# Performance work log

Hardware: AMD Instinct MI355X
Metric: run time of the kernel (lower is better)

## Reference

```python
import jax, jax.numpy as jnp
import numpy as np

HEADS = 4

def _pair_msg(H, w2, B, xsrc):
    # H:[E,mid] radial-MLP hidden; w2:[mid,co,ci,nf]; B:[E,m_out,m_in,nf] CG/SH basis; xsrc:[E,ci,m_in]
    tmp = jnp.einsum('epqf,eiq->eipf', B, xsrc)          # basis-weighted input  [E,ci,m_out,nf]
    R = jnp.einsum('eh,hoif->eoif', H, w2)               # per-edge radial weights [E,co,ci,nf]
    return jnp.einsum('eoif,eipf->eop', R, tmp)          # edge message [E,co,m_out]

def _conv_edges(ef, w1, w2_nf1, w2_11, b00, b01, b10, b11, x0s, x1s):
    # pair index p = 2*d_in + d_out; pairs (0,0),(0,1),(1,0) have nf=1, pair (1,1) has nf=3
    H = jax.nn.relu(jnp.einsum('ef,pfh->peh', ef, w1))
    m0 = _pair_msg(H[0], w2_nf1[0][..., None], b00, x0s) + _pair_msg(H[2], w2_nf1[2][..., None], b10, x1s)
    m1 = _pair_msg(H[1], w2_nf1[1][..., None], b01, x0s) + _pair_msg(H[3], w2_11, b11, x1s)
    return m0, m1

def _seg_softmax(z, dst, n):
    m = jax.ops.segment_max(z, dst, num_segments=n)
    m = jnp.where(jnp.isfinite(m), m, 0.0)
    e = jnp.exp(z - m[dst])
    s = jax.ops.segment_sum(e, dst, num_segments=n)
    return e / (s[dst] + 1e-9)

def _norm_se3(x, g, b, eps=1e-3):
    n = jnp.sqrt((x * x).sum(-1) + 1e-12)                # per-channel irrep norm [N,C]
    mu = n.mean(-1, keepdims=True)
    var = ((n - mu) ** 2).mean(-1, keepdims=True)
    ln = (n - mu) / jnp.sqrt(var + 1e-5) * g + b
    return x * (jax.nn.relu(ln) / (n + eps))[..., None]

def _forward(x0, x1, edge_feat, b00, b01, b10, b11, kv_w1, kv_w2_nf1, kv_w2_11,
             wq, wproj, norm_gamma, norm_beta, fc_w1, fc_w2_nf1, fc_w2_11, fc_wself,
             edge_src, edge_dst):
    N = x0.shape[0]
    E = edge_src.shape[0]
    L = kv_w1.shape[0]
    ckv = wq.shape[-1]
    scale = 1.0 / np.sqrt((ckv // HEADS) * 4)            # key feats per head over degrees 0,1 (1+3 comps)
    hs = lambda t: t.reshape(t.shape[0], HEADS, ckv // HEADS, t.shape[-1])
    for l in range(L):
        # AttentionBlockSE3: ConvSE3 -> per-edge key/value; LinearSE3 -> query; seg-softmax attention
        kv0, kv1 = _conv_edges(edge_feat, kv_w1[l], kv_w2_nf1[l], kv_w2_11[l],
                               b00, b01, b10, b11, x0[edge_src], x1[edge_src])
        k0, v0 = kv0[:, :ckv], kv0[:, ckv:]
        k1, v1 = kv1[:, :ckv], kv1[:, ckv:]
        q0 = jnp.einsum('ncm,cd->ndm', x0, wq[l, 0])
        q1 = jnp.einsum('ncm,cd->ndm', x1, wq[l, 1])
        z = (hs(q0)[edge_dst] * hs(k0)).sum((2, 3)) + (hs(q1)[edge_dst] * hs(k1)).sum((2, 3))
        alpha = _seg_softmax(z * scale, edge_dst, N)     # [E,heads]
        a0 = (alpha[:, :, None, None] * hs(v0)).reshape(E, ckv, 1)
        a1 = (alpha[:, :, None, None] * hs(v1)).reshape(E, ckv, 3)
        o0 = jax.ops.segment_sum(a0, edge_dst, num_segments=N)
        o1 = jax.ops.segment_sum(a1, edge_dst, num_segments=N)
        # project concat(attn_out, skip) per degree, then NormSE3
        x0 = jnp.einsum('ncm,cd->ndm', jnp.concatenate([o0, x0], 1), wproj[l, 0])
        x1 = jnp.einsum('ncm,cd->ndm', jnp.concatenate([o1, x1], 1), wproj[l, 1])
        x0 = _norm_se3(x0, norm_gamma[l, 0], norm_beta[l, 0])
        x1 = _norm_se3(x1, norm_gamma[l, 1], norm_beta[l, 1])
    # final ConvSE3 with self-interaction, scatter-aggregated over dst nodes
    m0, m1 = _conv_edges(edge_feat, fc_w1, fc_w2_nf1, fc_w2_11,
                         b00, b01, b10, b11, x0[edge_src], x1[edge_src])
    y0 = jax.ops.segment_sum(m0, edge_dst, num_segments=N) + jnp.einsum('ncm,cd->ndm', x0, fc_wself[0])
    y1 = jax.ops.segment_sum(m1, edge_dst, num_segments=N) + jnp.einsum('ncm,cd->ndm', x1, fc_wself[1])
    return jnp.concatenate([y0.reshape(N, -1), y1.reshape(N, -1)], axis=1)

def setup_inputs() -> dict:
    key = jax.random.key(0)
    ks = jax.random.split(key, 20)
    N, E, C, L = 8192, 131072, 16, 2
    Fe, mid, KV, ckv, Co = 16, 16, 16, 8, 8
    f = lambda k, s, sc=1.0: jax.random.normal(k, s, dtype=jnp.float32) * sc
    return {
        'x0': f(ks[0], (N, C, 1)),
        'x1': f(ks[1], (N, C, 3)),
        'edge_feat': f(ks[2], (E, Fe)),
        'b00': f(ks[3], (E, 1, 1, 1)),
        'b01': f(ks[4], (E, 3, 1, 1)),
        'b10': f(ks[5], (E, 1, 3, 1)),
        'b11': f(ks[6], (E, 3, 3, 3)),
        'kv_w1': f(ks[7], (L, 4, Fe, mid), 0.1),
        'kv_w2_nf1': f(ks[8], (L, 3, mid, KV, C), 0.1),
        'kv_w2_11': f(ks[9], (L, mid, KV, C, 3), 0.1),
        'wq': f(ks[10], (L, 2, C, ckv), 0.1),
        'wproj': f(ks[11], (L, 2, ckv + C, C), 0.1),
        'norm_gamma': jnp.ones((L, 2, C), dtype=jnp.float32),
        'norm_beta': jnp.zeros((L, 2, C), dtype=jnp.float32),
        'fc_w1': f(ks[12], (4, Fe, mid), 0.1),
        'fc_w2_nf1': f(ks[13], (3, mid, Co, C), 0.1),
        'fc_w2_11': f(ks[14], (mid, Co, C, 3), 0.1),
        'fc_wself': f(ks[15], (2, C, Co), 0.1),
        'edge_src': jax.random.randint(ks[16], (E,), 0, N, dtype=jnp.int32),
        'edge_dst': jax.random.randint(ks[17], (E,), 0, N, dtype=jnp.int32),
    }

def reference(x0, x1, edge_feat, b00, b01, b10, b11, kv_w1, kv_w2_nf1, kv_w2_11,
              wq, wproj, norm_gamma, norm_beta, fc_w1, fc_w2_nf1, fc_w2_11, fc_wself,
              edge_src, edge_dst):
    return _forward(x0, x1, edge_feat, b00, b01, b10, b11, kv_w1, kv_w2_nf1, kv_w2_11,
                    wq, wproj, norm_gamma, norm_beta, fc_w1, fc_w2_nf1, fc_w2_11, fc_wself,
                    edge_src, edge_dst)
```

## Files before the change

### kernel.cpp

```cpp
#include <hip/hip_runtime.h>
#include <hip/hip_bf16.h>
#include <math.h>


typedef short short8 __attribute__((ext_vector_type(8)));
typedef float f32x4 __attribute__((ext_vector_type(4)));

union ABfrag {
    short8 s8;
    __hip_bfloat162 b2[4];
};

static __device__ __forceinline__ unsigned short f2bf(float f) {
    unsigned x = __float_as_uint(f);
    unsigned r = x + 0x7FFFu + ((x >> 16) & 1u);
    return (unsigned short)(r >> 16);
}

__global__ void k_zero(int* p, int n) {
    int i = blockIdx.x * 256 + threadIdx.x;
    if (i < n) p[i] = 0;
}

__global__ void k_hist(const int* __restrict__ dst, int* __restrict__ counts, int E) {
    int e = blockIdx.x * 256 + threadIdx.x;
    if (e < E) atomicAdd(&counts[dst[e]], 1);
}

__global__ __launch_bounds__(1024) void k_scan(const int* __restrict__ counts,
                                               int* __restrict__ rowptr,
                                               int* __restrict__ cursor,
                                               int N, int CH) {
    __shared__ int part[1024];
    int t = threadIdx.x;
    int s = 0;
    for (int i = 0; i < CH; ++i) {
        int idx = t * CH + i;
        if (idx < N) s += counts[idx];
    }
    part[t] = s;
    __syncthreads();
    for (int off = 1; off < 1024; off <<= 1) {
        int v = (t >= off) ? part[t - off] : 0;
        __syncthreads();
        part[t] += v;
        __syncthreads();
    }
    int run = (t == 0) ? 0 : part[t - 1];
    for (int i = 0; i < CH; ++i) {
        int idx = t * CH + i;
        if (idx < N) {
            rowptr[idx] = run;
            cursor[idx] = run;
            run += counts[idx];
        }
    }
    if (t == 0) rowptr[N] = part[1023];
}

__global__ void k_scatter(const int* __restrict__ dst, int* __restrict__ cursor,
                          int* __restrict__ eids, int E) {
    int e = blockIdx.x * 256 + threadIdx.x;
    if (e < E) {
        int pos = atomicAdd(&cursor[dst[e]], 1);
        eids[pos] = e;
    }
}

__global__ void k_initx(const float* __restrict__ x0, const float* __restrict__ x1,
                        float* __restrict__ xs0, float* __restrict__ xs1, int n0, int n1) {
    int i = blockIdx.x * 256 + threadIdx.x;
    if (i < n0) xs0[i] = x0[i];
    else if (i < n0 + n1) xs1[i - n0] = x1[i - n0];
}

__global__ void k_efb(const float* __restrict__ ef, unsigned short* __restrict__ efb, int n) {
    int i = blockIdx.x * 256 + threadIdx.x;
    if (i < n) efb[i] = f2bf(ef[i]);
}

__global__ void k_prepw(const float* __restrict__ kvw1, const float* __restrict__ fcw1,
                        const float* __restrict__ kvw2n, const float* __restrict__ kvw211,
                        const float* __restrict__ fcw2n, const float* __restrict__ fcw211,
                        unsigned short* __restrict__ Wfrag) {
    int t = blockIdx.x * 256 + threadIdx.x;
    if (t >= 156 * 64 * 8) return;
    int j = t & 7;
    int lane = (t >> 3) & 63;
    int row = t >> 9;
    int quad = lane >> 4, m = lane & 15;
    int c = row / 52, r = row % 52;
    int KVO = (c < 2) ? 16 : 8;
    const float* w1src = (c < 2) ? (kvw1 + c * 1024) : fcw1;
    const float* w2n = (c < 2) ? (kvw2n + c * 12288) : fcw2n;
    const float* w211 = (c < 2) ? (kvw211 + c * 12288) : fcw211;
    float v = 0.f;
    if (r < 4) {
        if (quad < 2) v = w1src[r * 256 + (quad * 8 + j) * 16 + m];
    } else if (r < 28) {
        int fam = (r - 4) >> 3, kk = (r - 4) & 7;
        int h = quad * 4 + (j & 3), i = 2 * kk + (j >> 2);
        if (m < KVO) v = w2n[((fam * 16 + h) * KVO + m) * 16 + i];
    } else {
        int kk = r - 28;
        int h = quad * 4 + (j & 3);
        int ifx = 2 * kk + (j >> 2);
        int i = ifx / 3, f = ifx % 3;
        if (m < KVO) v = w211[((h * KVO + m) * 16 + i) * 3 + f];
    }
    Wfrag[t] = f2bf(v);
}

template <int KVO, bool DO_Z>
__global__ __launch_bounds__(256) void k_conv(
    int E,
    const int* __restrict__ src, const int* __restrict__ dst,
    const float* __restrict__ xs0, const float* __restrict__ xs1,
    const float* __restrict__ b00, const float* __restrict__ b01,
    const float* __restrict__ b10, const float* __restrict__ b11,
    const unsigned short* __restrict__ efb,
    const unsigned short* __restrict__ Wfrag,
    int base,
    const float* __restrict__ q0, const float* __restrict__ q1,
    float* __restrict__ out0, float* __restrict__ out1, float* __restrict__ zb)
{
    __shared__ float xBL[4][16 * 148];
    int tid = threadIdx.x;
    int wave = tid >> 6, lane = tid & 63;
    int tile = blockIdx.x * 4 + wave;
    if (tile * 16 >= E) return;
    int m = lane & 15, quad = lane >> 4;
    int e0 = tile * 16;
    int me = e0 + m;
    int s = src[me];
    float* xw = xBL[wave];
    const short8* W8 = (const short8*)Wfrag;

    {
        float x1c[12];
        const float4* xp = (const float4*)(xs1 + (size_t)s * 48 + quad * 12);
#pragma unroll
        for (int cc = 0; cc < 3; ++cc) {
            float4 v = xp[cc];
            x1c[cc * 4 + 0] = v.x; x1c[cc * 4 + 1] = v.y;
            x1c[cc * 4 + 2] = v.z; x1c[cc * 4 + 3] = v.w;
        }
        float b11r[27];
#pragma unroll
        for (int k = 0; k < 27; ++k) b11r[k] = b11[(size_t)me * 27 + k];
#pragma unroll
        for (int p = 0; p < 3; ++p) {
            float vals[12];
#pragma unroll
            for (int i2 = 0; i2 < 4; ++i2) {
#pragma unroll
                for (int f = 0; f < 3; ++f) {
                    float a = 0.f;
#pragma unroll
                    for (int q = 0; q < 3; ++q) a += x1c[i2 * 3 + q] * b11r[p * 9 + q * 3 + f];
                    vals[i2 * 3 + f] = a;
                }
            }
#pragma unroll
            for (int cc = 0; cc < 3; ++cc) {
                float4 v = make_float4(vals[cc * 4 + 0], vals[cc * 4 + 1],
                                       vals[cc * 4 + 2], vals[cc * 4 + 3]);
                *(float4*)&xw[m * 148 + p * 48 + quad * 12 + cc * 4] = v;
            }
        }
    }
    __syncthreads();

    float x0r[16];
    {
        const float4* p = (const float4*)(xs0 + (size_t)s * 16);
#pragma unroll
        for (int k = 0; k < 4; ++k) {
            float4 v = p[k];
            x0r[k * 4 + 0] = v.x; x0r[k * 4 + 1] = v.y;
            x0r[k * 4 + 2] = v.z; x0r[k * 4 + 3] = v.w;
        }
    }
    float t10[16];
    {
        float bq0 = b10[(size_t)me * 3 + 0], bq1 = b10[(size_t)me * 3 + 1],
              bq2 = b10[(size_t)me * 3 + 2];
        const float4* xp = (const float4*)(xs1 + (size_t)s * 48);
#pragma unroll
        for (int g = 0; g < 4; ++g) {
            float4 a = xp[g * 3 + 0], b = xp[g * 3 + 1], cc = xp[g * 3 + 2];
            float xf[12] = {a.x, a.y, a.z, a.w, b.x, b.y, b.z, b.w, cc.x, cc.y, cc.z, cc.w};
#pragma unroll
            for (int i2 = 0; i2 < 4; ++i2)
                t10[g * 4 + i2] = bq0 * xf[i2 * 3] + bq1 * xf[i2 * 3 + 1] + bq2 * xf[i2 * 3 + 2];
        }
    }

    float Hp[4][4];
    {
        short8 efr = {0, 0, 0, 0, 0, 0, 0, 0};
        if (quad < 2) efr = *(const short8*)(efb + (size_t)me * 16 + quad * 8);
        f32x4 z4 = {0.f, 0.f, 0.f, 0.f};
#pragma unroll
        for (int pp = 0; pp < 4; ++pp) {
            short8 w1f = W8[(size_t)(base + pp) * 64 + lane];
            f32x4 hacc = __builtin_amdgcn_mfma_f32_16x16x32_bf16(w1f, efr, z4, 0, 0, 0);
#pragma unroll
            for (int r = 0; r < 4; ++r) Hp[pp][r] = fmaxf(hacc[r], 0.f);
        }
    }

    f32x4 acc0 = {0.f, 0.f, 0.f, 0.f}, acc1 = acc0, acc2 = acc0;
    f32x4 accP0 = acc0, accP1 = acc0, accP2 = acc0;

#pragma unroll
    for (int kk = 0; kk < 8; ++kk) {
        float xa = x0r[2 * kk], xb_ = x0r[2 * kk + 1];
        float ta = t10[2 * kk], tb_ = t10[2 * kk + 1];
        ABfrag a0, a1, a2;
        a0.b2[0] = __float22bfloat162_rn(make_float2(Hp[0][0] * xa, Hp[0][1] * xa));
        a0.b2[1] = __float22bfloat162_rn(make_float2(Hp[0][2] * xa, Hp[0][3] * xa));
        a0.b2[2] = __float22bfloat162_rn(make_float2(Hp[0][0] * xb_, Hp[0][1] * xb_));
        a0.b2[3] = __float22bfloat162_rn(make_float2(Hp[0][2] * xb_, Hp[0][3] * xb_));
        a1.b2[0] = __float22bfloat162_rn(make_float2(Hp[1][0] * xa, Hp[1][1] * xa));
        a1.b2[1] = __float22bfloat162_rn(make_float2(Hp[1][2] * xa, Hp[1][3] * xa));
        a1.b2[2] = __float22bfloat162_rn(make_float2(Hp[1][0] * xb_, Hp[1][1] * xb_));
        a1.b2[3] = __float22bfloat162_rn(make_float2(Hp[1][2] * xb_, Hp[1][3] * xb_));
        a2.b2[0] = __float22bfloat162_rn(make_float2(Hp[2][0] * ta, Hp[2][1] * ta));
        a2.b2[1] = __float22bfloat162_rn(make_float2(Hp[2][2] * ta, Hp[2][3] * ta));
        a2.b2[2] = __float22bfloat162_rn(make_float2(Hp[2][0] * tb_, Hp[2][1] * tb_));
        a2.b2[3] = __float22bfloat162_rn(make_float2(Hp[2][2] * tb_, Hp[2][3] * tb_));
        short8 w0 = W8[(size_t)(base + 4 + kk) * 64 + lane];
        short8 w1f = W8[(size_t)(base + 4 + 8 + kk) * 64 + lane];
        short8 w2f = W8[(size_t)(base + 4 + 16 + kk) * 64 + lane];
        acc0 = __builtin_amdgcn_mfma_f32_16x16x32_bf16(w0, a0.s8, acc0, 0, 0, 0);
        acc1 = __builtin_amdgcn_mfma_f32_16x16x32_bf16(w1f, a1.s8, acc1, 0, 0, 0);
        acc2 = __builtin_amdgcn_mfma_f32_16x16x32_bf16(w2f, a2.s8, acc2, 0, 0, 0);
    }

#pragma unroll
    for (int kko = 0; kko < 12; ++kko) {
        float4 xb0 = *(const float4*)&xw[m * 148 + 0 * 48 + 4 * kko];
        float4 xb1 = *(const float4*)&xw[m * 148 + 1 * 48 + 4 * kko];
        float4 xb2 = *(const float4*)&xw[m * 148 + 2 * 48 + 4 * kko];
        float x0a[4] = {xb0.x, xb0.y, xb0.z, xb0.w};
        float x1a[4] = {xb1.x, xb1.y, xb1.z, xb1.w};
        float x2a[4] = {xb2.x, xb2.y, xb2.z, xb2.w};
#pragma unroll
        for (int t = 0; t < 2; ++t) {
            float p0a = x0a[2 * t], p0b = x0a[2 * t + 1];
            float p1a = x1a[2 * t], p1b = x1a[2 * t + 1];
            float p2a = x2a[2 * t], p2b = x2a[2 * t + 1];
            ABfrag a0, a1, a2;
            a0.b2[0] = __float22bfloat162_rn(make_float2(Hp[3][0] * p0a, Hp[3][1] * p0a));
            a0.b2[1] = __float22bfloat162_rn(make_float2(Hp[3][2] * p0a, Hp[3][3] * p0a));
            a0.b2[2] = __float22bfloat162_rn(make_float2(Hp[3][0] * p0b, Hp[3][1] * p0b));
            a0.b2[3] = __float22bfloat162_rn(make_float2(Hp[3][2] * p0b, Hp[3][3] * p0b));
            a1.b2[0] = __float22bfloat162_rn(make_float2(Hp[3][0] * p1a, Hp[3][1] * p1a));
            a1.b2[1] = __float22bfloat162_rn(make_float2(Hp[3][2] * p1a, Hp[3][3] * p1a));
            a1.b2[2] = __float22bfloat162_rn(make_float2(Hp[3][0] * p1b, Hp[3][1] * p1b));
            a1.b2[3] = __float22bfloat162_rn(make_float2(Hp[3][2] * p1b, Hp[3][3] * p1b));
            a2.b2[0] = __float22bfloat162_rn(make_float2(Hp[3][0] * p2a, Hp[3][1] * p2a));
            a2.b2[1] = __float22bfloat162_rn(make_float2(Hp[3][2] * p2a, Hp[3][3] * p2a));
            a2.b2[2] = __float22bfloat162_rn(make_float2(Hp[3][0] * p2b, Hp[3][1] * p2b));
            a2.b2[3] = __float22bfloat162_rn(make_float2(Hp[3][2] * p2b, Hp[3][3] * p2b));
            short8 wf = W8[(size_t)(base + 28 + 2 * kko + t) * 64 + lane];
            accP0 = __builtin_amdgcn_mfma_f32_16x16x32_bf16(wf, a0.s8, accP0, 0, 0, 0);
            accP1 = __builtin_amdgcn_mfma_f32_16x16x32_bf16(wf, a1.s8, accP1, 0, 0, 0);
            accP2 = __builtin_amdgcn_mfma_f32_16x16x32_bf16(wf, a2.s8, accP2, 0, 0, 0);
        }
    }

    float b00r = b00[me];
    float b01r0 = b01[(size_t)me * 3 + 0], b01r1 = b01[(size_t)me * 3 + 1],
          b01r2 = b01[(size_t)me * 3 + 2];
    float o0v[4], o1v[4][3];
#pragma unroll
    for (int r = 0; r < 4; ++r) {
        o0v[r] = b00r * acc0[r] + acc2[r];
        o1v[r][0] = b01r0 * acc1[r] + accP0[r];
        o1v[r][1] = b01r1 * acc1[r] + accP1[r];
        o1v[r][2] = b01r2 * acc1[r] + accP2[r];
    }
    bool doStore = DO_Z ? (quad >= 2) : (quad * 4 < KVO);
    if (doStore) {
        *(float4*)&out0[(size_t)me * KVO + quad * 4] =
            make_float4(o0v[0], o0v[1], o0v[2], o0v[3]);
        float* p1 = out1 + ((size_t)me * KVO + quad * 4) * 3;
        *(float4*)&p1[0] = make_float4(o1v[0][0], o1v[0][1], o1v[0][2], o1v[1][0]);
        *(float4*)&p1[4] = make_float4(o1v[1][1], o1v[1][2], o1v[2][0], o1v[2][1]);
        *(float4*)&p1[8] = make_float4(o1v[2][2], o1v[3][0], o1v[3][1], o1v[3][2]);
    }
    if (DO_Z && quad < 2) {
        int n = dst[me];
        float4 q0v = *(const float4*)&q0[(size_t)n * 8 + quad * 4];
        const float4* q1p = (const float4*)&q1[(size_t)n * 24 + quad * 12];
        float4 qa = q1p[0], qb = q1p[1], qc = q1p[2];
        float q1f[12] = {qa.x, qa.y, qa.z, qa.w, qb.x, qb.y, qb.z, qb.w,
                         qc.x, qc.y, qc.z, qc.w};
        float q0f[4] = {q0v.x, q0v.y, q0v.z, q0v.w};
        float zh0 = 0.f, zh1 = 0.f;
#pragma unroll
        for (int r = 0; r < 4; ++r) {
            float tt = q0f[r] * o0v[r] + q1f[r * 3 + 0] * o1v[r][0] +
                       q1f[r * 3 + 1] * o1v[r][1] + q1f[r * 3 + 2] * o1v[r][2];
            if (r < 2) zh0 += tt;
            else zh1 += tt;
        }
        const float scale = 0.35355339059327373f;
        *(float2*)&zb[(size_t)me * 4 + quad * 2] = make_float2(zh0 * scale, zh1 * scale);
    }
}

__global__ void k_q(int N, const float* __restrict__ xs0, const float* __restrict__ xs1,
                    const float* __restrict__ wq,
                    float* __restrict__ q0, float* __restrict__ q1) {
    int t = blockIdx.x * 256 + threadIdx.x;
    if (t >= N * 32) return;
    int n = t >> 5, comp = t & 31;
    if (comp < 8) {
        float a = 0.f;
#pragma unroll
        for (int c = 0; c < 16; ++c) a += xs0[n * 16 + c] * wq[c * 8 + comp];
        q0[n * 8 + comp] = a;
    } else {
        int idx = comp - 8, dd = idx / 3, mm = idx % 3;
        float a = 0.f;
#pragma unroll
        for (int c = 0; c < 16; ++c) a += xs1[n * 48 + c * 3 + mm] * wq[128 + c * 8 + dd];
        q1[n * 24 + dd * 3 + mm] = a;
    }
}

__global__ __launch_bounds__(256) void k_attn(
    int N,
    const int* __restrict__ rowptr, const int* __restrict__ eids,
    const float* __restrict__ z, const float* __restrict__ kv0, const float* __restrict__ kv1,
    const float* __restrict__ wproj,
    const float* __restrict__ gamma, const float* __restrict__ beta,
    float* __restrict__ xs0, float* __restrict__ xs1) {
    __shared__ float wpL[768];
    __shared__ float gL[32], btL[32];
    __shared__ float inb[16][100];
    int tid = threadIdx.x;
    for (int i = tid; i < 768; i += 256) wpL[i] = wproj[i];
    if (tid < 32) { gL[tid] = gamma[tid]; btL[tid] = beta[tid]; }
    int wave = tid >> 6, lane = tid & 63;
    int sub = lane >> 4, l16 = lane & 15;
    int nodeIdx = wave * 4 + sub;
    int n = blockIdx.x * 16 + nodeIdx;
    if (n >= N) n = N - 1;
    int base = rowptr[n], deg = rowptr[n + 1] - base;

    float mx0 = -INFINITY, mx1 = -INFINITY, mx2 = -INFINITY, mx3 = -INFINITY;
    for (int j = l16; j < deg; j += 16) {
        int e = eids[base + j];
        float4 zv = *(const float4*)&z[e * 4];
        mx0 = fmaxf(mx0, zv.x); mx1 = fmaxf(mx1, zv.y);
        mx2 = fmaxf(mx2, zv.z); mx3 = fmaxf(mx3, zv.w);
    }
#pragma unroll
    for (int off = 1; off < 16; off <<= 1) {
        mx0 = fmaxf(mx0, __shfl_xor(mx0, off));
        mx1 = fmaxf(mx1, __shfl_xor(mx1, off));
        mx2 = fmaxf(mx2, __shfl_xor(mx2, off));
        mx3 = fmaxf(mx3, __shfl_xor(mx3, off));
    }
    if (!isfinite(mx0)) mx0 = 0.f;
    if (!isfinite(mx1)) mx1 = 0.f;
    if (!isfinite(mx2)) mx2 = 0.f;
    if (!isfinite(mx3)) mx3 = 0.f;

    float s0 = 0.f, s1 = 0.f, s2 = 0.f, s3 = 0.f;
    for (int j = l16; j < deg; j += 16) {
        int e = eids[base + j];
        float4 zv = *(const float4*)&z[e * 4];
        s0 += __expf(zv.x - mx0); s1 += __expf(zv.y - mx1);
        s2 += __expf(zv.z - mx2); s3 += __expf(zv.w - mx3);
    }
#pragma unroll
    for (int off = 1; off < 16; off <<= 1) {
        s0 += __shfl_xor(s0, off); s1 += __shfl_xor(s1, off);
        s2 += __shfl_xor(s2, off); s3 += __shfl_xor(s3, off);
    }
    float mxa[4] = {mx0, mx1, mx2, mx3};
    float inva[4] = {1.f / (s0 + 1e-9f), 1.f / (s1 + 1e-9f),
                     1.f / (s2 + 1e-9f), 1.f / (s3 + 1e-9f)};

    int c0 = l16, c1 = l16 + 16;
    int kkA = c0 >> 3, dA = c0 & 7, hA = dA >> 1;
    int kkB = c1 >> 3, dB = c1 & 7, hB = dB >> 1;
    float mA = mxa[hA], iA = inva[hA];
    float mB = mxa[hB], iB = inva[hB];
    float accA = 0.f, accB = 0.f;
    for (int j = 0; j < deg; ++j) {
        int e = eids[base + j];
        float wA = __expf(z[e * 4 + hA] - mA) * iA;
        float wB = __expf(z[e * 4 + hB] - mB) * iB;
        float vA = (kkA == 0) ? kv0[(size_t)e * 16 + 8 + dA]
                              : kv1[((size_t)e * 16 + 8 + dA) * 3 + (kkA - 1)];
        float vB = kv1[((size_t)e * 16 + 8 + dB) * 3 + (kkB - 1)];
        accA += wA * vA;
        accB += wB * vB;
    }

    float* in0 = inb[nodeIdx];
    float* in1 = in0 + 24;
    if (c0 < 8) in0[c0] = accA;
    else in1[dA * 3 + (kkA - 1)] = accA;
    in1[dB * 3 + (kkB - 1)] = accB;
    in0[8 + l16] = xs0[(size_t)n * 16 + l16];
    {
        const float* xp = xs1 + (size_t)n * 48 + l16 * 3;
        in1[24 + l16 * 3 + 0] = xp[0];
        in1[24 + l16 * 3 + 1] = xp[1];
        in1[24 + l16 * 3 + 2] = xp[2];
    }
    __syncthreads();

    int c = l16;
    float y0 = 0.f;
#pragma unroll
    for (int j = 0; j < 24; ++j) y0 += in0[j] * wpL[j * 16 + c];
    float y1v[3];
#pragma unroll
    for (int mm = 0; mm < 3; ++mm) {
        float y = 0.f;
#pragma unroll
        for (int j = 0; j < 24; ++j) y += in1[j * 3 + mm] * wpL[384 + j * 16 + c];
        y1v[mm] = y;
    }
    float n0 = sqrtf(y0 * y0 + 1e-12f);
    float n1 = sqrtf(y1v[0] * y1v[0] + y1v[1] * y1v[1] + y1v[2] * y1v[2] + 1e-12f);
    float mu0 = n0, mu1 = n1;
#pragma unroll
    for (int off = 1; off < 16; off <<= 1) {
        mu0 += __shfl_xor(mu0, off);
        mu1 += __shfl_xor(mu1, off);
    }
    mu0 *= 0.0625f; mu1 *= 0.0625f;
    float dv0 = n0 - mu0, dv1 = n1 - mu1;
    float var0 = dv0 * dv0, var1 = dv1 * dv1;
#pragma unroll
    for (int off = 1; off < 16; off <<= 1) {
        var0 += __shfl_xor(var0, off);
        var1 += __shfl_xor(var1, off);
    }
    var0 *= 0.0625f; var1 *= 0.0625f;
    float ln0 = dv0 * rsqrtf(var0 + 1e-5f) * gL[c] + btL[c];
    float ln1 = dv1 * rsqrtf(var1 + 1e-5f) * gL[16 + c] + btL[16 + c];
    float fac0 = fmaxf(ln0, 0.f) / (n0 + 1e-3f);
    float fac1 = fmaxf(ln1, 0.f) / (n1 + 1e-3f);
    xs0[(size_t)n * 16 + c] = y0 * fac0;
    float* xo = xs1 + (size_t)n * 48 + c * 3;
    xo[0] = y1v[0] * fac1;
    xo[1] = y1v[1] * fac1;
    xo[2] = y1v[2] * fac1;
}

__global__ __launch_bounds__(256) void k_out(
    int N,
    const int* __restrict__ rowptr, const int* __restrict__ eids,
    const float* __restrict__ m0f, const float* __restrict__ m1f,
    const float* __restrict__ xs0, const float* __restrict__ xs1,
    const float* __restrict__ wself,
    float* __restrict__ out) {
    int tid = threadIdx.x;
    int wave = tid >> 6, lane = tid & 63;
    int sub = lane >> 4, l16 = lane & 15;
    int n = blockIdx.x * 16 + wave * 4 + sub;
    if (n >= N) n = N - 1;
    int base = rowptr[n], deg = rowptr[n + 1] - base;

    int c0 = l16, c1 = l16 + 16;
    int kkA = c0 >> 3, dA = c0 & 7;
    int kkB = c1 >> 3, dB = c1 & 7;
    float accA = 0.f, accB = 0.f;
    for (int j = 0; j < deg; ++j) {
        int e = eids[base + j];
        accA += (kkA == 0) ? m0f[(size_t)e * 8 + dA]
                           : m1f[((size_t)e * 8 + dA) * 3 + (kkA - 1)];
        accB += m1f[((size_t)e * 8 + dB) * 3 + (kkB - 1)];
    }
    if (kkA == 0) {
#pragma unroll
        for (int c = 0; c < 16; ++c) accA += xs0[(size_t)n * 16 + c] * wself[c * 8 + dA];
    } else {
#pragma unroll
        for (int c = 0; c < 16; ++c)
            accA += xs1[(size_t)n * 48 + c * 3 + (kkA - 1)] * wself[128 + c * 8 + dA];
    }
    {
        int mm = kkB - 1;
#pragma unroll
        for (int c = 0; c < 16; ++c)
            accB += xs1[(size_t)n * 48 + c * 3 + mm] * wself[128 + c * 8 + dB];
    }
    out[(size_t)n * 32 + ((kkA == 0) ? dA : (8 + dA * 3 + (kkA - 1)))] = accA;
    out[(size_t)n * 32 + (8 + dB * 3 + (kkB - 1))] = accB;
}

extern "C" void kernel_launch(void* const* d_in, const int* in_sizes, int n_in,
                              void* d_out, int out_size, void* d_ws, size_t ws_size,
                              hipStream_t stream) {
    const float* x0 = (const float*)d_in[0];
    const float* x1 = (const float*)d_in[1];
    const float* ef = (const float*)d_in[2];
    const float* b00 = (const float*)d_in[3];
    const float* b01 = (const float*)d_in[4];
    const float* b10 = (const float*)d_in[5];
    const float* b11 = (const float*)d_in[6];
    const float* kvw1 = (const float*)d_in[7];
    const float* kvw2n = (const float*)d_in[8];
    const float* kvw211 = (const float*)d_in[9];
    const float* wq = (const float*)d_in[10];
    const float* wproj = (const float*)d_in[11];
    const float* gam = (const float*)d_in[12];
    const float* bet = (const float*)d_in[13];
    const float* fcw1 = (const float*)d_in[14];
    const float* fcw2n = (const float*)d_in[15];
    const float* fcw211 = (const float*)d_in[16];
    const float* fcself = (const float*)d_in[17];
    const int* esrc = (const int*)d_in[18];
    const int* edst = (const int*)d_in[19];
    int N = in_sizes[0] / 16;
    int E = in_sizes[18];
    float* out = (float*)d_out;

    float* ws = (float*)d_ws;
    size_t off = 0;
    float* xs0 = ws + off; off += (size_t)N * 16;
    float* xs1 = ws + off; off += (size_t)N * 48;
    float* q0b = ws + off; off += (size_t)N * 8;
    float* q1b = ws + off; off += (size_t)N * 24;
    float* kv0 = ws + off; off += (size_t)E * 16;
    float* kv1 = ws + off; off += (size_t)E * 48;
    float* zb = ws + off; off += (size_t)E * 4;
    int* counts = (int*)(ws + off); off += N;
    int* rowptr = (int*)(ws + off); off += N + 1;
    int* cursor = (int*)(ws + off); off += N;
    int* eids = (int*)(ws + off); off += E;
    off = (off + 3) & ~(size_t)3;
    unsigned short* efb = (unsigned short*)(ws + off); off += (size_t)E * 16 / 2;
    unsigned short* Wfrag = (unsigned short*)(ws + off); off += (size_t)156 * 64 * 8 / 2;

    const int tpb = 256;
    int ebl = (E + 255) / 256;
    int cblk = (E / 16 + 3) / 4;
    int nbl16 = (N + 15) / 16;

    k_prepw<<<(156 * 512 + 255) / 256, tpb, 0, stream>>>(kvw1, fcw1, kvw2n, kvw211,
                                                         fcw2n, fcw211, Wfrag);
    k_efb<<<(E * 16 + 255) / 256, tpb, 0, stream>>>(ef, efb, E * 16);
    k_zero<<<(N + 255) / 256, tpb, 0, stream>>>(counts, N);
    k_hist<<<ebl, tpb, 0, stream>>>(edst, counts, E);
    int CH = (N + 1023) / 1024;
    k_scan<<<1, 1024, 0, stream>>>(counts, rowptr, cursor, N, CH);
    k_scatter<<<ebl, tpb, 0, stream>>>(edst, cursor, eids, E);
    k_initx<<<(N * 64 + 255) / 256, tpb, 0, stream>>>(x0, x1, xs0, xs1, N * 16, N * 48);

    for (int l = 0; l < 2; ++l) {
        k_q<<<(N * 32 + 255) / 256, tpb, 0, stream>>>(N, xs0, xs1, wq + l * 256, q0b, q1b);
        k_conv<16, true><<<cblk, tpb, 0, stream>>>(E, esrc, edst, xs0, xs1, b00, b01, b10, b11,
                                                   efb, Wfrag, l * 52, q0b, q1b, kv0, kv1, zb);
        k_attn<<<nbl16, tpb, 0, stream>>>(N, rowptr, eids, zb, kv0, kv1,
                                          wproj + l * 768, gam + l * 32, bet + l * 32, xs0, xs1);
    }
    k_conv<8, false><<<cblk, tpb, 0, stream>>>(E, esrc, edst, xs0, xs1, b00, b01, b10, b11,
                                               efb, Wfrag, 2 * 52, q0b, q1b, kv0, kv1, zb);
    k_out<<<nbl16, tpb, 0, stream>>>(N, rowptr, eids, kv0, kv1, xs0, xs1, fcself, out);
}
```

Measured before the change: 354.4 us.

## Switch conv to fp16 packed math and store values in dst-sorted rows

The conv kernel now builds its MFMA operands with packed fp16 multiplies and f16 MFMA instead of fp32 multiplies followed by bf16 conversion. It also writes only the value part of each message into a CSR-ordered 32-float row per edge, using a per-edge position from the scatter step. The attention and output kernels therefore read contiguous rows with no edge-id indirection, and attention stages its softmax weights in shared memory. Small setup kernels are merged and a memset replaces the zero kernel. fp16 has a narrower range than bf16, so values could overflow or lose precision.

```diff
diff --git a/kernel.cpp b/kernel.cpp
--- a/kernel.cpp
+++ b/kernel.cpp
@@ -1,26 +1,19 @@
 #include <hip/hip_runtime.h>
-#include <hip/hip_bf16.h>
+#include <hip/hip_fp16.h>
 #include <math.h>
 
 
-typedef short short8 __attribute__((ext_vector_type(8)));
+typedef _Float16 half8 __attribute__((ext_vector_type(8)));
 typedef float f32x4 __attribute__((ext_vector_type(4)));
 
-union ABfrag {
-    short8 s8;
-    __hip_bfloat162 b2[4];
+union AF {
+    half8 h8;
+    __half2 h2[4];
 };
-
-static __device__ __forceinline__ unsigned short f2bf(float f) {
-    unsigned x = __float_as_uint(f);
-    unsigned r = x + 0x7FFFu + ((x >> 16) & 1u);
-    return (unsigned short)(r >> 16);
-}
-
-__global__ void k_zero(int* p, int n) {
-    int i = blockIdx.x * 256 + threadIdx.x;
-    if (i < n) p[i] = 0;
-}
+union U32h2 {
+    unsigned u;
+    __half2 h;
+};
 
 __global__ void k_hist(const int* __restrict__ dst, int* __restrict__ counts, int E) {
     int e = blockIdx.x * 256 + threadIdx.x;
@@ -59,24 +52,25 @@
 }
 
 __global__ void k_scatter(const int* __restrict__ dst, int* __restrict__ cursor,
-                          int* __restrict__ eids, int E) {
+                          int* __restrict__ pose, int E) {
     int e = blockIdx.x * 256 + threadIdx.x;
     if (e < E) {
         int pos = atomicAdd(&cursor[dst[e]], 1);
-        eids[pos] = e;
-    }
-}
-
-__global__ void k_initx(const float* __restrict__ x0, const float* __restrict__ x1,
-                        float* __restrict__ xs0, float* __restrict__ xs1, int n0, int n1) {
+        pose[e] = pos;
+    }
+}
+
+__global__ void k_misc(const float* __restrict__ x0, const float* __restrict__ x1,
+                       const float* __restrict__ ef,
+                       float* __restrict__ xs0, float* __restrict__ xs1,
+                       unsigned short* __restrict__ efh, int n0, int n1, int n2) {
     int i = blockIdx.x * 256 + threadIdx.x;
     if (i < n0) xs0[i] = x0[i];
     else if (i < n0 + n1) xs1[i - n0] = x1[i - n0];
-}
-
-__global__ void k_efb(const float* __restrict__ ef, unsigned short* __restrict__ efb, int n) {
-    int i = blockIdx.x * 256 + threadIdx.x;
-    if (i < n) efb[i] = f2bf(ef[i]);
+    else if (i < n0 + n1 + n2) {
+        int k = i - n0 - n1;
+        efh[k] = __half_as_ushort(__float2half(ef[k]));
+    }
 }
 
 __global__ void k_prepw(const float* __restrict__ kvw1, const float* __restrict__ fcw1,
@@ -108,23 +102,24 @@
         int i = ifx / 3, f = ifx % 3;
         if (m < KVO) v = w211[((h * KVO + m) * 16 + i) * 3 + f];
     }
-    Wfrag[t] = f2bf(v);
+    Wfrag[t] = __half_as_ushort(__float2half(v));
 }
 
 template <int KVO, bool DO_Z>
 __global__ __launch_bounds__(256) void k_conv(
     int E,
     const int* __restrict__ src, const int* __restrict__ dst,
+    const int* __restrict__ pose,
     const float* __restrict__ xs0, const float* __restrict__ xs1,
     const float* __restrict__ b00, const float* __restrict__ b01,
     const float* __restrict__ b10, const float* __restrict__ b11,
-    const unsigned short* __restrict__ efb,
+    const unsigned short* __restrict__ efh,
     const unsigned short* __restrict__ Wfrag,
-    int base,
+    int wbase,
     const float* __restrict__ q0, const float* __restrict__ q1,
-    float* __restrict__ out0, float* __restrict__ out1, float* __restrict__ zb)
+    float* __restrict__ vrow, float* __restrict__ zb)
 {
-    __shared__ float xBL[4][16 * 148];
+    __shared__ unsigned xBL[4][16 * 148];
     int tid = threadIdx.x;
     int wave = tid >> 6, lane = tid & 63;
     int tile = blockIdx.x * 4 + wave;
@@ -133,8 +128,8 @@
     int e0 = tile * 16;
     int me = e0 + m;
     int s = src[me];
-    float* xw = xBL[wave];
-    const short8* W8 = (const short8*)Wfrag;
+    unsigned* xw = xBL[wave];
+    const half8* W8 = (const half8*)Wfrag;
 
     {
         float x1c[12];
@@ -163,26 +158,31 @@
             }
 #pragma unroll
             for (int cc = 0; cc < 3; ++cc) {
-                float4 v = make_float4(vals[cc * 4 + 0], vals[cc * 4 + 1],
-                                       vals[cc * 4 + 2], vals[cc * 4 + 3]);
-                *(float4*)&xw[m * 148 + p * 48 + quad * 12 + cc * 4] = v;
+                unsigned uu[4];
+#pragma unroll
+                for (int i3 = 0; i3 < 4; ++i3) {
+                    U32h2 u;
+                    u.h = __float2half2_rn(vals[cc * 4 + i3]);
+                    uu[i3] = u.u;
+                }
+                *(uint4*)&xw[m * 148 + p * 48 + quad * 12 + cc * 4] =
+                    make_uint4(uu[0], uu[1], uu[2], uu[3]);
             }
         }
     }
     __syncthreads();
 
-    float x0r[16];
+    __half2 x0d[16], t10d[16];
     {
         const float4* p = (const float4*)(xs0 + (size_t)s * 16);
 #pragma unroll
         for (int k = 0; k < 4; ++k) {
             float4 v = p[k];
-            x0r[k * 4 + 0] = v.x; x0r[k * 4 + 1] = v.y;
-            x0r[k * 4 + 2] = v.z; x0r[k * 4 + 3] = v.w;
-        }
-    }
-    float t10[16];
-    {
+            x0d[k * 4 + 0] = __float2half2_rn(v.x);
+            x0d[k * 4 + 1] = __float2half2_rn(v.y);
+            x0d[k * 4 + 2] = __float2half2_rn(v.z);
+            x0d[k * 4 + 3] = __float2half2_rn(v.w);
+        }
         float bq0 = b10[(size_t)me * 3 + 0], bq1 = b10[(size_t)me * 3 + 1],
               bq2 = b10[(size_t)me * 3 + 2];
         const float4* xp = (const float4*)(xs1 + (size_t)s * 48);
@@ -192,21 +192,24 @@
             float xf[12] = {a.x, a.y, a.z, a.w, b.x, b.y, b.z, b.w, cc.x, cc.y, cc.z, cc.w};
 #pragma unroll
             for (int i2 = 0; i2 < 4; ++i2)
-                t10[g * 4 + i2] = bq0 * xf[i2 * 3] + bq1 * xf[i2 * 3 + 1] + bq2 * xf[i2 * 3 + 2];
-        }
-    }
-
-    float Hp[4][4];
+                t10d[g * 4 + i2] = __float2half2_rn(
+                    bq0 * xf[i2 * 3] + bq1 * xf[i2 * 3 + 1] + bq2 * xf[i2 * 3 + 2]);
+        }
+    }
+
+    __half2 Hp2[4][2];
     {
-        short8 efr = {0, 0, 0, 0, 0, 0, 0, 0};
-        if (quad < 2) efr = *(const short8*)(efb + (size_t)me * 16 + quad * 8);
+        half8 efr = {0, 0, 0, 0, 0, 0, 0, 0};
+        if (quad < 2) efr = *(const half8*)(efh + (size_t)me * 16 + quad * 8);
         f32x4 z4 = {0.f, 0.f, 0.f, 0.f};
 #pragma unroll
         for (int pp = 0; pp < 4; ++pp) {
-            short8 w1f = W8[(size_t)(base + pp) * 64 + lane];
-            f32x4 hacc = __builtin_amdgcn_mfma_f32_16x16x32_bf16(w1f, efr, z4, 0, 0, 0);
-#pragma unroll
-            for (int r = 0; r < 4; ++r) Hp[pp][r] = fmaxf(hacc[r], 0.f);
+            half8 w1f = W8[(size_t)(wbase + pp) * 64 + lane];
+            f32x4 hacc = __builtin_amdgcn_mfma_f32_16x16x32_f16(w1f, efr, z4, 0, 0, 0);
+            Hp2[pp][0] = __float22half2_rn(
+                make_float2(fmaxf(hacc[0], 0.f), fmaxf(hacc[1], 0.f)));
+            Hp2[pp][1] = __float22half2_rn(
+                make_float2(fmaxf(hacc[2], 0.f), fmaxf(hacc[3], 0.f)));
         }
     }
 
@@ -215,59 +218,49 @@
 
 #pragma unroll
     for (int kk = 0; kk < 8; ++kk) {
-        float xa = x0r[2 * kk], xb_ = x0r[2 * kk + 1];
-        float ta = t10[2 * kk], tb_ = t10[2 * kk + 1];
-        ABfrag a0, a1, a2;
-        a0.b2[0] = __float22bfloat162_rn(make_float2(Hp[0][0] * xa, Hp[0][1] * xa));
-        a0.b2[1] = __float22bfloat162_rn(make_float2(Hp[0][2] * xa, Hp[0][3] * xa));
-        a0.b2[2] = __float22bfloat162_rn(make_float2(Hp[0][0] * xb_, Hp[0][1] * xb_));
-        a0.b2[3] = __float22bfloat162_rn(make_float2(Hp[0][2] * xb_, Hp[0][3] * xb_));
-        a1.b2[0] = __float22bfloat162_rn(make_float2(Hp[1][0] * xa, Hp[1][1] * xa));
-        a1.b2[1] = __float22bfloat162_rn(make_float2(Hp[1][2] * xa, Hp[1][3] * xa));
-        a1.b2[2] = __float22bfloat162_rn(make_float2(Hp[1][0] * xb_, Hp[1][1] * xb_));
-        a1.b2[3] = __float22bfloat162_rn(make_float2(Hp[1][2] * xb_, Hp[1][3] * xb_));
-        a2.b2[0] = __float22bfloat162_rn(make_float2(Hp[2][0] * ta, Hp[2][1] * ta));
-        a2.b2[1] = __float22bfloat162_rn(make_float2(Hp[2][2] * ta, Hp[2][3] * ta));
-        a2.b2[2] = __float22bfloat162_rn(make_float2(Hp[2][0] * tb_, Hp[2][1] * tb_));
-        a2.b2[3] = __float22bfloat162_rn(make_float2(Hp[2][2] * tb_, Hp[2][3] * tb_));
-        short8 w0 = W8[(size_t)(base + 4 + kk) * 64 + lane];
-        short8 w1f = W8[(size_t)(base + 4 + 8 + kk) * 64 + lane];
-        short8 w2f = W8[(size_t)(base + 4 + 16 + kk) * 64 + lane];
-        acc0 = __builtin_amdgcn_mfma_f32_16x16x32_bf16(w0, a0.s8, acc0, 0, 0, 0);
-        acc1 = __builtin_amdgcn_mfma_f32_16x16x32_bf16(w1f, a1.s8, acc1, 0, 0, 0);
-        acc2 = __builtin_amdgcn_mfma_f32_16x16x32_bf16(w2f, a2.s8, acc2, 0, 0, 0);
+        __half2 xA = x0d[2 * kk], xB = x0d[2 * kk + 1];
+        __half2 tA = t10d[2 * kk], tB = t10d[2 * kk + 1];
+        AF a0, a1, a2;
+        a0.h2[0] = __hmul2(Hp2[0][0], xA); a0.h2[1] = __hmul2(Hp2[0][1], xA);
+        a0.h2[2] = __hmul2(Hp2[0][0], xB); a0.h2[3] = __hmul2(Hp2[0][1], xB);
+        a1.h2[0] = __hmul2(Hp2[1][0], xA); a1.h2[1] = __hmul2(Hp2[1][1], xA);
+        a1.h2[2] = __hmul2(Hp2[1][0], xB); a1.h2[3] = __hmul2(Hp2[1][1], xB);
+        a2.h2[0] = __hmul2(Hp2[2][0], tA); a2.h2[1] = __hmul2(Hp2[2][1], tA);
+        a2.h2[2] = __hmul2(Hp2[2][0], tB); a2.h2[3] = __hmul2(Hp2[2][1], tB);
+        half8 w0 = W8[(size_t)(wbase + 4 + kk) * 64 + lane];
+        half8 w1f = W8[(size_t)(wbase + 12 + kk) * 64 + lane];
+        half8 w2f = W8[(size_t)(wbase + 20 + kk) * 64 + lane];
+        acc0 = __builtin_amdgcn_mfma_f32_16x16x32_f16(w0, a0.h8, acc0, 0, 0, 0);
+        acc1 = __builtin_amdgcn_mfma_f32_16x16x32_f16(w1f, a1.h8, acc1, 0, 0, 0);
+        acc2 = __builtin_amdgcn_mfma_f32_16x16x32_f16(w2f, a2.h8, acc2, 0, 0, 0);
     }
 
 #pragma unroll
     for (int kko = 0; kko < 12; ++kko) {
-        float4 xb0 = *(const float4*)&xw[m * 148 + 0 * 48 + 4 * kko];
-        float4 xb1 = *(const float4*)&xw[m * 148 + 1 * 48 + 4 * kko];
-        float4 xb2 = *(const float4*)&xw[m * 148 + 2 * 48 + 4 * kko];
-        float x0a[4] = {xb0.x, xb0.y, xb0.z, xb0.w};
-        float x1a[4] = {xb1.x, xb1.y, xb1.z, xb1.w};
-        float x2a[4] = {xb2.x, xb2.y, xb2.z, xb2.w};
+        uint4 xu0 = *(const uint4*)&xw[m * 148 + 0 * 48 + 4 * kko];
+        uint4 xu1 = *(const uint4*)&xw[m * 148 + 1 * 48 + 4 * kko];
+        uint4 xu2 = *(const uint4*)&xw[m * 148 + 2 * 48 + 4 * kko];
+        unsigned qa0[4] = {xu0.x, xu0.y, xu0.z, xu0.w};
+        unsigned qa1[4] = {xu1.x, xu1.y, xu1.z, xu1.w};
+        unsigned qa2[4] = {xu2.x, xu2.y, xu2.z, xu2.w};
 #pragma unroll
         for (int t = 0; t < 2; ++t) {
-            float p0a = x0a[2 * t], p0b = x0a[2 * t + 1];
-            float p1a = x1a[2 * t], p1b = x1a[2 * t + 1];
-            float p2a = x2a[2 * t], p2b = x2a[2 * t + 1];
-            ABfrag a0, a1, a2;
-            a0.b2[0] = __float22bfloat162_rn(make_float2(Hp[3][0] * p0a, Hp[3][1] * p0a));
-            a0.b2[1] = __float22bfloat162_rn(make_float2(Hp[3][2] * p0a, Hp[3][3] * p0a));
-            a0.b2[2] = __float22bfloat162_rn(make_float2(Hp[3][0] * p0b, Hp[3][1] * p0b));
-            a0.b2[3] = __float22bfloat162_rn(make_float2(Hp[3][2] * p0b, Hp[3][3] * p0b));
-            a1.b2[0] = __float22bfloat162_rn(make_float2(Hp[3][0] * p1a, Hp[3][1] * p1a));
-            a1.b2[1] = __float22bfloat162_rn(make_float2(Hp[3][2] * p1a, Hp[3][3] * p1a));
-            a1.b2[2] = __float22bfloat162_rn(make_float2(Hp[3][0] * p1b, Hp[3][1] * p1b));
-            a1.b2[3] = __float22bfloat162_rn(make_float2(Hp[3][2] * p1b, Hp[3][3] * p1b));
-            a2.b2[0] = __float22bfloat162_rn(make_float2(Hp[3][0] * p2a, Hp[3][1] * p2a));
-            a2.b2[1] = __float22bfloat162_rn(make_float2(Hp[3][2] * p2a, Hp[3][3] * p2a));
-            a2.b2[2] = __float22bfloat162_rn(make_float2(Hp[3][0] * p2b, Hp[3][1] * p2b));
-            a2.b2[3] = __float22bfloat162_rn(make_float2(Hp[3][2] * p2b, Hp[3][3] * p2b));
-            short8 wf = W8[(size_t)(base + 28 + 2 * kko + t) * 64 + lane];
-            accP0 = __builtin_amdgcn_mfma_f32_16x16x32_bf16(wf, a0.s8, accP0, 0, 0, 0);
-            accP1 = __builtin_amdgcn_mfma_f32_16x16x32_bf16(wf, a1.s8, accP1, 0, 0, 0);
-            accP2 = __builtin_amdgcn_mfma_f32_16x16x32_bf16(wf, a2.s8, accP2, 0, 0, 0);
+            U32h2 u;
+            __half2 p0a, p0b, p1a, p1b, p2a, p2b;
+            u.u = qa0[2 * t]; p0a = u.h; u.u = qa0[2 * t + 1]; p0b = u.h;
+            u.u = qa1[2 * t]; p1a = u.h; u.u = qa1[2 * t + 1]; p1b = u.h;
+            u.u = qa2[2 * t]; p2a = u.h; u.u = qa2[2 * t + 1]; p2b = u.h;
+            AF a0, a1, a2;
+            a0.h2[0] = __hmul2(Hp2[3][0], p0a); a0.h2[1] = __hmul2(Hp2[3][1], p0a);
+            a0.h2[2] = __hmul2(Hp2[3][0], p0b); a0.h2[3] = __hmul2(Hp2[3][1], p0b);
+            a1.h2[0] = __hmul2(Hp2[3][0], p1a); a1.h2[1] = __hmul2(Hp2[3][1], p1a);
+            a1.h2[2] = __hmul2(Hp2[3][0], p1b); a1.h2[3] = __hmul2(Hp2[3][1], p1b);
+            a2.h2[0] = __hmul2(Hp2[3][0], p2a); a2.h2[1] = __hmul2(Hp2[3][1], p2a);
+            a2.h2[2] = __hmul2(Hp2[3][0], p2b); a2.h2[3] = __hmul2(Hp2[3][1], p2b);
+            half8 wf = W8[(size_t)(wbase + 28 + 2 * kko + t) * 64 + lane];
+            accP0 = __builtin_amdgcn_mfma_f32_16x16x32_f16(wf, a0.h8, accP0, 0, 0, 0);
+            accP1 = __builtin_amdgcn_mfma_f32_16x16x32_f16(wf, a1.h8, accP1, 0, 0, 0);
+            accP2 = __builtin_amdgcn_mfma_f32_16x16x32_f16(wf, a2.h8, accP2, 0, 0, 0);
         }
     }
 
@@ -282,11 +275,13 @@
         o1v[r][1] = b01r1 * acc1[r] + accP1[r];
         o1v[r][2] = b01r2 * acc1[r] + accP2[r];
     }
-    bool doStore = DO_Z ? (quad >= 2) : (quad * 4 < KVO);
+    int pos = pose[me];
+    bool doStore = DO_Z ? (quad >= 2) : (quad < 2);
     if (doStore) {
-        *(float4*)&out0[(size_t)me * KVO + quad * 4] =
-            make_float4(o0v[0], o0v[1], o0v[2], o0v[3]);
-        float* p1 = out1 + ((size_t)me * KVO + quad * 4) * 3;
+        int qa = DO_Z ? (quad - 2) : quad;
+        float* vp = vrow + (size_t)pos * 32;
+        *(float4*)&vp[qa * 4] = make_float4(o0v[0], o0v[1], o0v[2], o0v[3]);
+        float* p1 = vp + 8 + qa * 12;
         *(float4*)&p1[0] = make_float4(o1v[0][0], o1v[0][1], o1v[0][2], o1v[1][0]);
         *(float4*)&p1[4] = make_float4(o1v[1][1], o1v[1][2], o1v[2][0], o1v[2][1]);
         *(float4*)&p1[8] = make_float4(o1v[2][2], o1v[3][0], o1v[3][1], o1v[3][2]);
@@ -295,9 +290,9 @@
         int n = dst[me];
         float4 q0v = *(const float4*)&q0[(size_t)n * 8 + quad * 4];
         const float4* q1p = (const float4*)&q1[(size_t)n * 24 + quad * 12];
-        float4 qa = q1p[0], qb = q1p[1], qc = q1p[2];
-        float q1f[12] = {qa.x, qa.y, qa.z, qa.w, qb.x, qb.y, qb.z, qb.w,
-                         qc.x, qc.y, qc.z, qc.w};
+        float4 qa4 = q1p[0], qb4 = q1p[1], qc4 = q1p[2];
+        float q1f[12] = {qa4.x, qa4.y, qa4.z, qa4.w, qb4.x, qb4.y, qb4.z, qb4.w,
+                         qc4.x, qc4.y, qc4.z, qc4.w};
         float q0f[4] = {q0v.x, q0v.y, q0v.z, q0v.w};
         float zh0 = 0.f, zh1 = 0.f;
 #pragma unroll
@@ -308,7 +303,7 @@
             else zh1 += tt;
         }
         const float scale = 0.35355339059327373f;
-        *(float2*)&zb[(size_t)me * 4 + quad * 2] = make_float2(zh0 * scale, zh1 * scale);
+        *(float2*)&zb[(size_t)pos * 4 + quad * 2] = make_float2(zh0 * scale, zh1 * scale);
     }
 }
 
@@ -334,14 +329,15 @@
 
 __global__ __launch_bounds__(256) void k_attn(
     int N,
-    const int* __restrict__ rowptr, const int* __restrict__ eids,
-    const float* __restrict__ z, const float* __restrict__ kv0, const float* __restrict__ kv1,
+    const int* __restrict__ rowptr,
+    const float* __restrict__ zb, const float* __restrict__ vrow,
     const float* __restrict__ wproj,
     const float* __restrict__ gamma, const float* __restrict__ beta,
     float* __restrict__ xs0, float* __restrict__ xs1) {
     __shared__ float wpL[768];
     __shared__ float gL[32], btL[32];
     __shared__ float inb[16][100];
+    __shared__ float aw[16][16][4];
     int tid = threadIdx.x;
     for (int i = tid; i < 768; i += 256) wpL[i] = wproj[i];
     if (tid < 32) { gL[tid] = gamma[tid]; btL[tid] = beta[tid]; }
@@ -351,11 +347,11 @@
     int n = blockIdx.x * 16 + nodeIdx;
     if (n >= N) n = N - 1;
     int base = rowptr[n], deg = rowptr[n + 1] - base;
+    const float4* zb4 = (const float4*)zb;
 
     float mx0 = -INFINITY, mx1 = -INFINITY, mx2 = -INFINITY, mx3 = -INFINITY;
     for (int j = l16; j < deg; j += 16) {
-        int e = eids[base + j];
-        float4 zv = *(const float4*)&z[e * 4];
+        float4 zv = zb4[base + j];
         mx0 = fmaxf(mx0, zv.x); mx1 = fmaxf(mx1, zv.y);
         mx2 = fmaxf(mx2, zv.z); mx3 = fmaxf(mx3, zv.w);
     }
@@ -373,8 +369,7 @@
 
     float s0 = 0.f, s1 = 0.f, s2 = 0.f, s3 = 0.f;
     for (int j = l16; j < deg; j += 16) {
-        int e = eids[base + j];
-        float4 zv = *(const float4*)&z[e * 4];
+        float4 zv = zb4[base + j];
         s0 += __expf(zv.x - mx0); s1 += __expf(zv.y - mx1);
         s2 += __expf(zv.z - mx2); s3 += __expf(zv.w - mx3);
     }
@@ -383,32 +378,38 @@
         s0 += __shfl_xor(s0, off); s1 += __shfl_xor(s1, off);
         s2 += __shfl_xor(s2, off); s3 += __shfl_xor(s3, off);
     }
-    float mxa[4] = {mx0, mx1, mx2, mx3};
-    float inva[4] = {1.f / (s0 + 1e-9f), 1.f / (s1 + 1e-9f),
-                     1.f / (s2 + 1e-9f), 1.f / (s3 + 1e-9f)};
-
-    int c0 = l16, c1 = l16 + 16;
-    int kkA = c0 >> 3, dA = c0 & 7, hA = dA >> 1;
-    int kkB = c1 >> 3, dB = c1 & 7, hB = dB >> 1;
-    float mA = mxa[hA], iA = inva[hA];
-    float mB = mxa[hB], iB = inva[hB];
+    float i0 = 1.f / (s0 + 1e-9f), i1 = 1.f / (s1 + 1e-9f);
+    float i2 = 1.f / (s2 + 1e-9f), i3 = 1.f / (s3 + 1e-9f);
+
+    int c0 = 2 * l16, c1 = c0 + 1;
+    int hA = ((c0 < 8) ? c0 : (c0 - 8) / 3) >> 1;
+    int hB = ((c1 < 8) ? c1 : (c1 - 8) / 3) >> 1;
     float accA = 0.f, accB = 0.f;
-    for (int j = 0; j < deg; ++j) {
-        int e = eids[base + j];
-        float wA = __expf(z[e * 4 + hA] - mA) * iA;
-        float wB = __expf(z[e * 4 + hB] - mB) * iB;
-        float vA = (kkA == 0) ? kv0[(size_t)e * 16 + 8 + dA]
-                              : kv1[((size_t)e * 16 + 8 + dA) * 3 + (kkA - 1)];
-        float vB = kv1[((size_t)e * 16 + 8 + dB) * 3 + (kkB - 1)];
-        accA += wA * vA;
-        accB += wB * vB;
+    for (int j0 = 0; j0 < deg; j0 += 16) {
+        int j = j0 + l16;
+        float4 a4 = make_float4(0.f, 0.f, 0.f, 0.f);
+        if (j < deg) {
+            float4 zv = zb4[base + j];
+            a4.x = __expf(zv.x - mx0) * i0;
+            a4.y = __expf(zv.y - mx1) * i1;
+            a4.z = __expf(zv.z - mx2) * i2;
+            a4.w = __expf(zv.w - mx3) * i3;
+        }
+        *(float4*)&aw[nodeIdx][l16][0] = a4;
+        __builtin_amdgcn_wave_barrier();
+        int cnt = min(16, deg - j0);
+        for (int jj = 0; jj < cnt; ++jj) {
+            float2 v = *(const float2*)&vrow[(size_t)(base + j0 + jj) * 32 + c0];
+            accA += aw[nodeIdx][jj][hA] * v.x;
+            accB += aw[nodeIdx][jj][hB] * v.y;
+        }
+        __builtin_amdgcn_wave_barrier();
     }
 
     float* in0 = inb[nodeIdx];
     float* in1 = in0 + 24;
-    if (c0 < 8) in0[c0] = accA;
-    else in1[dA * 3 + (kkA - 1)] = accA;
-    in1[dB * 3 + (kkB - 1)] = accB;
+    if (c0 < 8) { in0[c0] = accA; in0[c1] = accB; }
+    else        { in1[c0 - 8] = accA; in1[c1 - 8] = accB; }
     in0[8 + l16] = xs0[(size_t)n * 16 + l16];
     {
         const float* xp = xs1 + (size_t)n * 48 + l16 * 3;
@@ -460,8 +461,7 @@
 
 __global__ __launch_bounds__(256) void k_out(
     int N,
-    const int* __restrict__ rowptr, const int* __restrict__ eids,
-    const float* __restrict__ m0f, const float* __restrict__ m1f,
+    const int* __restrict__ rowptr, const float* __restrict__ vrow,
     const float* __restrict__ xs0, const float* __restrict__ xs1,
     const float* __restrict__ wself,
     float* __restrict__ out) {
@@ -472,32 +472,30 @@
     if (n >= N) n = N - 1;
     int base = rowptr[n], deg = rowptr[n + 1] - base;
 
-    int c0 = l16, c1 = l16 + 16;
-    int kkA = c0 >> 3, dA = c0 & 7;
-    int kkB = c1 >> 3, dB = c1 & 7;
+    int c0 = 2 * l16, c1 = c0 + 1;
     float accA = 0.f, accB = 0.f;
     for (int j = 0; j < deg; ++j) {
-        int e = eids[base + j];
-        accA += (kkA == 0) ? m0f[(size_t)e * 8 + dA]
-                           : m1f[((size_t)e * 8 + dA) * 3 + (kkA - 1)];
-        accB += m1f[((size_t)e * 8 + dB) * 3 + (kkB - 1)];
-    }
-    if (kkA == 0) {
-#pragma unroll
-        for (int c = 0; c < 16; ++c) accA += xs0[(size_t)n * 16 + c] * wself[c * 8 + dA];
+        float2 v = *(const float2*)&vrow[(size_t)(base + j) * 32 + c0];
+        accA += v.x;
+        accB += v.y;
+    }
+    if (c0 < 8) {
+#pragma unroll
+        for (int c = 0; c < 16; ++c) {
+            float xv = xs0[(size_t)n * 16 + c];
+            accA += xv * wself[c * 8 + c0];
+            accB += xv * wself[c * 8 + c1];
+        }
     } else {
-#pragma unroll
-        for (int c = 0; c < 16; ++c)
-            accA += xs1[(size_t)n * 48 + c * 3 + (kkA - 1)] * wself[128 + c * 8 + dA];
-    }
-    {
-        int mm = kkB - 1;
-#pragma unroll
-        for (int c = 0; c < 16; ++c)
-            accB += xs1[(size_t)n * 48 + c * 3 + mm] * wself[128 + c * 8 + dB];
-    }
-    out[(size_t)n * 32 + ((kkA == 0) ? dA : (8 + dA * 3 + (kkA - 1)))] = accA;
-    out[(size_t)n * 32 + (8 + dB * 3 + (kkB - 1))] = accB;
+        int dA = (c0 - 8) / 3, mA = (c0 - 8) % 3;
+        int dB = (c1 - 8) / 3, mB = (c1 - 8) % 3;
+#pragma unroll
+        for (int c = 0; c < 16; ++c) {
+            accA += xs1[(size_t)n * 48 + c * 3 + mA] * wself[128 + c * 8 + dA];
+            accB += xs1[(size_t)n * 48 + c * 3 + mB] * wself[128 + c * 8 + dB];
+        }
+    }
+    *(float2*)&out[(size_t)n * 32 + c0] = make_float2(accA, accB);
 }
 
 extern "C" void kernel_launch(void* const* d_in, const int* in_sizes, int n_in,
@@ -533,15 +531,14 @@
     float* xs1 = ws + off; off += (size_t)N * 48;
     float* q0b = ws + off; off += (size_t)N * 8;
     float* q1b = ws + off; off += (size_t)N * 24;
-    float* kv0 = ws + off; off += (size_t)E * 16;
-    float* kv1 = ws + off; off += (size_t)E * 48;
+    float* vrow = ws + off; off += (size_t)E * 32;
     float* zb = ws + off; off += (size_t)E * 4;
     int* counts = (int*)(ws + off); off += N;
     int* rowptr = (int*)(ws + off); off += N + 1;
     int* cursor = (int*)(ws + off); off += N;
-    int* eids = (int*)(ws + off); off += E;
+    int* pose = (int*)(ws + off); off += E;
     off = (off + 3) & ~(size_t)3;
-    unsigned short* efb = (unsigned short*)(ws + off); off += (size_t)E * 16 / 2;
+    unsigned short* efh = (unsigned short*)(ws + off); off += (size_t)E * 16 / 2;
     unsigned short* Wfrag = (unsigned short*)(ws + off); off += (size_t)156 * 64 * 8 / 2;
 
     const int tpb = 256;
@@ -551,22 +548,25 @@
 
     k_prepw<<<(156 * 512 + 255) / 256, tpb, 0, stream>>>(kvw1, fcw1, kvw2n, kvw211,
                                                          fcw2n, fcw211, Wfrag);
-    k_efb<<<(E * 16 + 255) / 256, tpb, 0, stream>>>(ef, efb, E * 16);
-    k_zero<<<(N + 255) / 256, tpb, 0, stream>>>(counts, N);
+    int mtot = N * 64 + E * 16;
+    k_misc<<<(mtot + 255) / 256, tpb, 0, stream>>>(x0, x1, ef, xs0, xs1, efh,
+                                                   N * 16, N * 48, E * 16);
+    hipMemsetAsync(counts, 0, (size_t)N * 4, stream);
     k_hist<<<ebl, tpb, 0, stream>>>(edst, counts, E);
     int CH = (N + 1023) / 1024;
     k_scan<<<1, 1024, 0, stream>>>(counts, rowptr, cursor, N, CH);
-    k_scatter<<<ebl, tpb, 0, stream>>>(edst, cursor, eids, E);
-    k_initx<<<(N * 64 + 255) / 256, tpb, 0, stream>>>(x0, x1, xs0, xs1, N * 16, N * 48);
+    k_scatter<<<ebl, tpb, 0, stream>>>(edst, cursor, pose, E);
 
     for (int l = 0; l < 2; ++l) {
         k_q<<<(N * 32 + 255) / 256, tpb, 0, stream>>>(N, xs0, xs1, wq + l * 256, q0b, q1b);
-        k_conv<16, true><<<cblk, tpb, 0, stream>>>(E, esrc, edst, xs0, xs1, b00, b01, b10, b11,
-                                                   efb, Wfrag, l * 52, q0b, q1b, kv0, kv1, zb);
-        k_attn<<<nbl16, tpb, 0, stream>>>(N, rowptr, eids, zb, kv0, kv1,
-                                          wproj + l * 768, gam + l * 32, bet + l * 32, xs0, xs1);
-    }
-    k_conv<8, false><<<cblk, tpb, 0, stream>>>(E, esrc, edst, xs0, xs1, b00, b01, b10, b11,
-                                               efb, Wfrag, 2 * 52, q0b, q1b, kv0, kv1, zb);
-    k_out<<<nbl16, tpb, 0, stream>>>(N, rowptr, eids, kv0, kv1, xs0, xs1, fcself, out);
-}
+        k_conv<16, true><<<cblk, tpb, 0, stream>>>(E, esrc, edst, pose, xs0, xs1,
+                                                   b00, b01, b10, b11, efh, Wfrag, l * 52,
+                                                   q0b, q1b, vrow, zb);
+        k_attn<<<nbl16, tpb, 0, stream>>>(N, rowptr, zb, vrow, wproj + l * 768,
+                                          gam + l * 32, bet + l * 32, xs0, xs1);
+    }
+    k_conv<8, false><<<cblk, tpb, 0, stream>>>(E, esrc, edst, pose, xs0, xs1,
+                                               b00, b01, b10, b11, efh, Wfrag, 2 * 52,
+                                               q0b, q1b, vrow, zb);
+    k_out<<<nbl16, tpb, 0, stream>>>(N, rowptr, vrow, xs0, xs1, fcself, out);
+}
```

After: 295.2 us. -16.7%, faster.
